# Kernel tuning notes

Measured on AMD Instinct MI355X. Metric: run time of the kernel, lower is better.

## Reference

```python
import jax, jax.numpy as jnp
import numpy as np

N_EMBD = 2048
N_HEAD = 16
HEAD_DIM = N_EMBD // N_HEAD
B, T = 8, 1024
EPS = 1e-5


def setup_inputs() -> dict:
    key = jax.random.key(0)
    ks = jax.random.split(key, 8)
    s = 0.02
    return {
        "x": jax.random.normal(ks[0], (B, T, N_EMBD), dtype=jnp.float32),
        "ln1_w": jnp.ones((N_EMBD,), jnp.float32),
        "ln1_b": jnp.zeros((N_EMBD,), jnp.float32),
        "qkv_w": jax.random.normal(ks[1], (3 * N_EMBD, N_EMBD), jnp.float32) * s,
        "qkv_b": jnp.zeros((3 * N_EMBD,), jnp.float32),
        "out_w": jax.random.normal(ks[2], (N_EMBD, N_EMBD), jnp.float32) * s,
        "out_b": jnp.zeros((N_EMBD,), jnp.float32),
        "ln2_w": jnp.ones((N_EMBD,), jnp.float32),
        "ln2_b": jnp.zeros((N_EMBD,), jnp.float32),
        "fc1_w": jax.random.normal(ks[3], (4 * N_EMBD, N_EMBD), jnp.float32) * s,
        "fc1_b": jnp.zeros((4 * N_EMBD,), jnp.float32),
        "fc2_w": jax.random.normal(ks[4], (N_EMBD, 4 * N_EMBD), jnp.float32) * s,
        "fc2_b": jnp.zeros((N_EMBD,), jnp.float32),
    }


def _layernorm(x, w, b):
    mu = jnp.mean(x, axis=-1, keepdims=True)
    var = jnp.var(x, axis=-1, keepdims=True)
    return (x - mu) * jax.lax.rsqrt(var + EPS) * w + b


def _attention(x, qkv_w, qkv_b, out_w, out_b):
    Bb, Tt, C = x.shape
    qkv = x @ qkv_w.T + qkv_b                      # [B,T,3C]
    q, k, v = jnp.split(qkv, 3, axis=-1)
    def heads(t):  # [B,T,C] -> [B,H,T,D]
        return t.reshape(Bb, Tt, N_HEAD, HEAD_DIM).transpose(0, 2, 1, 3)
    q, k, v = heads(q), heads(k), heads(v)
    scale = 1.0 / np.sqrt(HEAD_DIM).astype(np.float32)
    scores = jnp.einsum('bhqd,bhkd->bhqk', q, k) * scale
    causal = jnp.tril(jnp.ones((Tt, Tt), dtype=bool))
    scores = jnp.where(causal, scores, -jnp.inf)
    attn = jax.nn.softmax(scores, axis=-1)         # dropout p=0 -> identity
    out = jnp.einsum('bhqk,bhkd->bhqd', attn, v)
    out = out.transpose(0, 2, 1, 3).reshape(Bb, Tt, C)
    return out @ out_w.T + out_b


def _mlp(x, fc1_w, fc1_b, fc2_w, fc2_b):
    h = jax.nn.gelu(x @ fc1_w.T + fc1_b, approximate=False)  # torch GELU is exact erf
    return h @ fc2_w.T + fc2_b


def reference(x, ln1_w, ln1_b, qkv_w, qkv_b, out_w, out_b,
              ln2_w, ln2_b, fc1_w, fc1_b, fc2_w, fc2_b):
    x = x + _attention(_layernorm(x, ln1_w, ln1_b), qkv_w, qkv_b, out_w, out_b)
    x = x + _mlp(_layernorm(x, ln2_w, ln2_b), fc1_w, fc1_b, fc2_w, fc2_b)
    return x
```

## Files before the change

kernel.cpp:

```cpp
#include <hip/hip_runtime.h>
#include <hip/hip_bf16.h>

typedef __attribute__((ext_vector_type(8))) short short8;
typedef __attribute__((ext_vector_type(4))) short short4v;
typedef __attribute__((ext_vector_type(4))) float f32x4;
typedef __attribute__((address_space(3))) char lds_char;

static __device__ __forceinline__ ushort f2bf(float f) {
  union { __hip_bfloat16 h; ushort u; } cv;
  cv.h = __float2bfloat16(f);
  return cv.u;
}

#define GLOAD_LDS16(gp, lp)                                            \
  __builtin_amdgcn_global_load_lds(                                    \
      (const __attribute__((address_space(1))) void*)(gp),             \
      (__attribute__((address_space(3))) void*)(lp), 16, 0, 0)

#define BAR   asm volatile("s_barrier" ::: "memory")
#define VM0   asm volatile("s_waitcnt vmcnt(0)" ::: "memory")
#define LGKM0_SB do { asm volatile("s_waitcnt lgkmcnt(0)" ::: "memory");  \
                      __builtin_amdgcn_sched_barrier(0); } while (0)

__global__ __launch_bounds__(256) void cvt_all_k(const float* __restrict__ w0, ushort* __restrict__ o0, int n0,
                                                 const float* __restrict__ w1, ushort* __restrict__ o1, int n1,
                                                 const float* __restrict__ w2, ushort* __restrict__ o2, int n2,
                                                 const float* __restrict__ w3, ushort* __restrict__ o3, int n3) {
  int i = blockIdx.x * 256 + threadIdx.x;
  const float* in; ushort* out;
  if (i < n0)           { in = w0; out = o0; }
  else if (i < n0 + n1) { i -= n0; in = w1; out = o1; }
  else if (i < n0 + n1 + n2) { i -= n0 + n1; in = w2; out = o2; }
  else                  { i -= n0 + n1 + n2; if (i >= n3) return; in = w3; out = o3; }
  const float4* p = (const float4*)in + (size_t)i * 2;
  float4 a = p[0], b = p[1];
  short8 o;
  o[0] = f2bf(a.x); o[1] = f2bf(a.y); o[2] = f2bf(a.z); o[3] = f2bf(a.w);
  o[4] = f2bf(b.x); o[5] = f2bf(b.y); o[6] = f2bf(b.z); o[7] = f2bf(b.w);
  ((short8*)out)[i] = o;
}

__global__ __launch_bounds__(256) void ln_k(const float* __restrict__ x, const float* __restrict__ w,
                                            const float* __restrict__ b, ushort* __restrict__ o) {
  const int row = blockIdx.x, t = threadIdx.x;
  const float* xr = x + (size_t)row * 2048;
  float4 v0 = *(const float4*)(xr + t * 4);
  float4 v1 = *(const float4*)(xr + t * 4 + 1024);
  float s  = v0.x + v0.y + v0.z + v0.w + v1.x + v1.y + v1.z + v1.w;
  float s2 = v0.x*v0.x + v0.y*v0.y + v0.z*v0.z + v0.w*v0.w
           + v1.x*v1.x + v1.y*v1.y + v1.z*v1.z + v1.w*v1.w;
  #pragma unroll
  for (int m = 32; m; m >>= 1) { s += __shfl_xor(s, m); s2 += __shfl_xor(s2, m); }
  __shared__ float red[8];
  const int lane = t & 63, wv = t >> 6;
  if (lane == 0) { red[wv * 2] = s; red[wv * 2 + 1] = s2; }
  __syncthreads();
  s  = red[0] + red[2] + red[4] + red[6];
  s2 = red[1] + red[3] + red[5] + red[7];
  const float mu = s * (1.f / 2048.f);
  const float rstd = rsqrtf(s2 * (1.f / 2048.f) - mu * mu + 1e-5f);
  float4 w0 = *(const float4*)(w + t * 4), w1 = *(const float4*)(w + t * 4 + 1024);
  float4 b0 = *(const float4*)(b + t * 4), b1 = *(const float4*)(b + t * 4 + 1024);
  short4v o0, o1;
  o0[0] = f2bf((v0.x - mu) * rstd * w0.x + b0.x);
  o0[1] = f2bf((v0.y - mu) * rstd * w0.y + b0.y);
  o0[2] = f2bf((v0.z - mu) * rstd * w0.z + b0.z);
  o0[3] = f2bf((v0.w - mu) * rstd * w0.w + b0.w);
  o1[0] = f2bf((v1.x - mu) * rstd * w1.x + b1.x);
  o1[1] = f2bf((v1.y - mu) * rstd * w1.y + b1.y);
  o1[2] = f2bf((v1.z - mu) * rstd * w1.z + b1.z);
  o1[3] = f2bf((v1.w - mu) * rstd * w1.w + b1.w);
  *(short4v*)(o + (size_t)row * 2048 + t * 4) = o0;
  *(short4v*)(o + (size_t)row * 2048 + t * 4 + 1024) = o1;
}

template <int EPI>
__global__ __launch_bounds__(512, 4) void gemm256_k(const ushort* __restrict__ A, const ushort* __restrict__ B,
                                                    const float* __restrict__ bias, const float* __restrict__ res,
                                                    void* __restrict__ outp, int M, int N, int K) {
  __shared__ __align__(16) char lds[49152];
  const int nbn = N >> 7;
  const int nwg = gridDim.x;
  const int cpx = nwg >> 3;
  const int bid = (blockIdx.x & 7) * cpx + (blockIdx.x >> 3);
  const int gsz = nbn << 2;
  const int g = bid / gsz, rr = bid % gsz;
  const int bm = (g << 2) + (rr & 3), bn = rr >> 2;
  const int m0 = bm << 8, n0 = bn << 7;
  const int t = threadIdx.x, lane = t & 63, wid = t >> 6;
  const int wr = wid >> 2, wcn = wid & 3;
  const int hi = lane >> 4, lo = lane & 15;
  const int srow = lane >> 3, sc8 = lane & 7;
  const int gcs = (sc8 ^ srow) * 8;
  const ushort* Abase = A + (size_t)m0 * K;
  const ushort* Bbase = B + (size_t)n0 * K;
  f32x4 acc[8][2] = {};

  auto stageA = [&](int h, int tt) {
    const size_t kof = (size_t)tt * 64 + gcs;
    #pragma unroll
    for (int j = 0; j < 2; j++) {
      const int rb = h * 128 + wid * 16 + j * 8;
      GLOAD_LDS16(Abase + (size_t)(rb + srow) * K + kof, (ushort*)(lds + rb * 128));
    }
  };
  auto stageB = [&](int tt) {
    const size_t kof = (size_t)tt * 64 + gcs;
    #pragma unroll
    for (int j = 0; j < 2; j++) {
      const int rb = wid * 16 + j * 8;
      GLOAD_LDS16(Bbase + (size_t)(rb + srow) * K + kof, (ushort*)(lds + 32768 + rb * 128));
    }
  };

  const int swz = (lo & 7) << 4;
  const char* LA = lds;
  const char* LB = lds + 32768;
  const int arow0 = wr * 128 + lo;
  const int brow0 = wcn * 32 + lo;

  const int NT = K >> 6;
  stageA(0, 0); stageA(1, 0); stageB(0);

  for (int tt = 0; tt < NT; ++tt) {
    VM0; BAR;
    __builtin_amdgcn_s_setprio(1);
    #pragma unroll
    for (int kk = 0; kk < 2; kk++) {
      const int cb = kk * 64 + hi * 16;
      short8 bb0 = *(const short8*)(LB + (brow0 + 0)  * 128 + (cb ^ swz));
      short8 bb1 = *(const short8*)(LB + (brow0 + 16) * 128 + (cb ^ swz));
      #pragma unroll
      for (int m = 0; m < 8; m++) {
        short8 af = *(const short8*)(LA + (arow0 + m * 16) * 128 + (cb ^ swz));
        acc[m][0] = __builtin_amdgcn_mfma_f32_16x16x32_bf16(af, bb0, acc[m][0], 0, 0, 0);
        acc[m][1] = __builtin_amdgcn_mfma_f32_16x16x32_bf16(af, bb1, acc[m][1], 0, 0, 0);
      }
    }
    __builtin_amdgcn_s_setprio(0);
    BAR;
    if (tt + 1 < NT) { stageA(0, tt + 1); stageA(1, tt + 1); stageB(tt + 1); }
  }

  #pragma unroll
  for (int m = 0; m < 8; m++) {
    const int grow = m0 + wr * 128 + m * 16 + hi * 4;
    #pragma unroll
    for (int ni = 0; ni < 2; ni++) {
      const int gcol = n0 + wcn * 32 + ni * 16 + lo;
      const float bv = bias[gcol];
      #pragma unroll
      for (int r = 0; r < 4; r++) {
        const size_t idx = (size_t)(grow + r) * N + gcol;
        float v = acc[m][ni][r] + bv;
        if constexpr (EPI == 0) ((ushort*)outp)[idx] = f2bf(v);
        else if constexpr (EPI == 1) ((float*)outp)[idx] = res[idx] + v;
        else if constexpr (EPI == 2) ((ushort*)outp)[idx] = f2bf(0.5f * v * (1.f + erff(v * 0.70710678118f)));
        else ((float*)outp)[idx] += v;
      }
    }
  }
}

__global__ __launch_bounds__(256) void attn_k(const ushort* __restrict__ qkv, ushort* __restrict__ o) {
  const int qb = 15 - blockIdx.y;
  const int bh = blockIdx.x;
  const int bb = bh >> 4, h = bh & 15;
  const int t = threadIdx.x, lane = t & 63, w = t >> 6;
  const int hi = lane >> 4, lo = lane & 15;
  __shared__ __align__(16) char ldsK[64 * 256];
  __shared__ __align__(16) char ldsV[64 * 256];
  __shared__ __align__(16) char ldsP[4][16 * 128];
  const size_t base = (size_t)bb * 1024 * 6144;
  const int qrow_a = qb * 64 + w * 16 + lo;
  short8 qf[4];
  #pragma unroll
  for (int kk = 0; kk < 4; kk++)
    qf[kk] = *(const short8*)(qkv + base + (size_t)qrow_a * 6144 + h * 128 + kk * 32 + hi * 8);
  float ms[4], ls[4];
  f32x4 oacc[8] = {};
  #pragma unroll
  for (int r = 0; r < 4; r++) { ms[r] = -1e30f; ls[r] = 0.f; }
  const int wave_qmax = qb * 64 + w * 16 + 15;
  const uint vbase = (uint)(size_t)(lds_char*)ldsV + hi * 2048 + lo * 8;
  const int k_r4  = lane >> 4;
  const int v_kv4 = (lane >> 1) & 3;
  const int v_d0  = (lane >> 3) * 16 + (lane & 1) * 8;

  for (int kv0 = 0; kv0 <= qb * 64; kv0 += 64) {
    __syncthreads();
    #pragma unroll
    for (int j = 0; j < 4; j++) {
      const int rb = w * 16 + j * 4;
      const int r  = rb + k_r4;
      const int c16 = (lane & 15) ^ (r & 7);
      GLOAD_LDS16(qkv + base + (size_t)(kv0 + r) * 6144 + 2048 + h * 128 + c16 * 8,
                  ldsK + rb * 256);
    }
    #pragma unroll
    for (int j = 0; j < 4; j++) {
      const int g = w * 4 + j;
      GLOAD_LDS16(qkv + base + (size_t)(kv0 + g * 4 + v_kv4) * 6144 + 4096 + h * 128 + v_d0,
                  ldsV + g * 1024);
    }
    __syncthreads();
    if (kv0 > wave_qmax) continue;
    f32x4 s[4];
    #pragma unroll
    for (int nb = 0; nb < 4; nb++) {
      f32x4 z = {};
      const int krow = nb * 16 + lo;
      #pragma unroll
      for (int kk = 0; kk < 4; kk++) {
        const int cb = kk * 64 + hi * 16;
        short8 kf = *(const short8*)(ldsK + krow * 256 + (cb ^ ((krow & 7) << 4)));
        z = __builtin_amdgcn_mfma_f32_16x16x32_bf16(qf[kk], kf, z, 0, 0, 0);
      }
      s[nb] = z;
    }
    float corr[4];
    #pragma unroll
    for (int r = 0; r < 4; r++) {
      const int qrow = qb * 64 + w * 16 + hi * 4 + r;
      float mx = -1e30f;
      #pragma unroll
      for (int nb = 0; nb < 4; nb++) {
        const int kcol = kv0 + nb * 16 + lo;
        float sv = s[nb][r] * 0.08838834764831845f;
        sv = (kcol <= qrow) ? sv : -1e30f;
        s[nb][r] = sv;
        mx = fmaxf(mx, sv);
      }
      #pragma unroll
      for (int msk = 1; msk < 16; msk <<= 1) mx = fmaxf(mx, __shfl_xor(mx, msk));
      const float mnew = fmaxf(ms[r], mx);
      corr[r] = __expf(ms[r] - mnew);
      ms[r] = mnew;
      float rs = 0.f;
      #pragma unroll
      for (int nb = 0; nb < 4; nb++) {
        const float p = __expf(s[nb][r] - mnew);
        s[nb][r] = p; rs += p;
      }
      #pragma unroll
      for (int msk = 1; msk < 16; msk <<= 1) rs += __shfl_xor(rs, msk);
      ls[r] = ls[r] * corr[r] + rs;
    }
    #pragma unroll
    for (int nf = 0; nf < 8; nf++)
      #pragma unroll
      for (int r = 0; r < 4; r++) oacc[nf][r] *= corr[r];
    #pragma unroll
    for (int r = 0; r < 4; r++) {
      const int prow = hi * 4 + r;
      #pragma unroll
      for (int nb = 0; nb < 4; nb++) {
        const int pcol = nb * 16 + lo;
        *(short*)(ldsP[w] + prow * 128 + ((pcol * 2) ^ ((prow & 7) << 4))) = (short)f2bf(s[nb][r]);
      }
    }
    #pragma unroll
    for (int ks = 0; ks < 2; ks++) {
      short8 pf = *(const short8*)(ldsP[w] + lo * 128 + ((ks * 64 + hi * 16) ^ ((lo & 7) << 4)));
      short4v v0[8], v1[8];
      #pragma unroll
      for (int nf = 0; nf < 8; nf++) {
        const uint a0 = vbase + ks * 8192 + nf * 128;
        asm volatile("ds_read_b64_tr_b16 %0, %1" : "=v"(v0[nf]) : "v"(a0));
        asm volatile("ds_read_b64_tr_b16 %0, %1" : "=v"(v1[nf]) : "v"(a0 + 1024));
      }
      LGKM0_SB;
      #pragma unroll
      for (int nf = 0; nf < 8; nf++) {
        short8 vf = __builtin_shufflevector(v0[nf], v1[nf], 0, 1, 2, 3, 4, 5, 6, 7);
        oacc[nf] = __builtin_amdgcn_mfma_f32_16x16x32_bf16(pf, vf, oacc[nf], 0, 0, 0);
      }
    }
  }
  #pragma unroll
  for (int r = 0; r < 4; r++) {
    const float inv = 1.f / ls[r];
    const int qrow = qb * 64 + w * 16 + hi * 4 + r;
    ushort* orow = o + ((size_t)(bb * 1024 + qrow)) * 2048 + h * 128;
    #pragma unroll
    for (int nf = 0; nf < 8; nf++)
      orow[nf * 16 + lo] = f2bf(oacc[nf][r] * inv);
  }
}

extern "C" void kernel_launch(void* const* d_in, const int* in_sizes, int n_in,
                              void* d_out, int out_size, void* d_ws, size_t ws_size,
                              hipStream_t stream) {
  const float* x     = (const float*)d_in[0];
  const float* ln1w  = (const float*)d_in[1];
  const float* ln1b  = (const float*)d_in[2];
  const float* qkvw  = (const float*)d_in[3];
  const float* qkvb  = (const float*)d_in[4];
  const float* outw  = (const float*)d_in[5];
  const float* outb  = (const float*)d_in[6];
  const float* ln2w  = (const float*)d_in[7];
  const float* ln2b  = (const float*)d_in[8];
  const float* fc1w  = (const float*)d_in[9];
  const float* fc1b  = (const float*)d_in[10];
  const float* fc2w  = (const float*)d_in[11];
  const float* fc2b  = (const float*)d_in[12];
  float* out = (float*)d_out;

  char* ws = (char*)d_ws;
  ushort* qkvw_bf = (ushort*)(ws);
  ushort* outw_bf = (ushort*)(ws + 25165824);
  ushort* fc1w_bf = (ushort*)(ws + 33554432);
  ushort* fc2w_bf = (ushort*)(ws + 67108864);
  ushort* bufA    = (ushort*)(ws + 100663296);
  ushort* bufR    = (ushort*)(ws + 134217728);

  cvt_all_k<<<24576, 256, 0, stream>>>(qkvw, qkvw_bf, 1572864,
                                       outw, outw_bf, 524288,
                                       fc1w, fc1w_bf, 2097152,
                                       fc2w, fc2w_bf, 2097152);

  ln_k<<<8192, 256, 0, stream>>>(x, ln1w, ln1b, bufA);
  gemm256_k<0><<<1536, 512, 0, stream>>>(bufA, qkvw_bf, qkvb, nullptr, bufR, 8192, 6144, 2048);
  attn_k<<<dim3(128, 16), 256, 0, stream>>>(bufR, bufA);
  gemm256_k<1><<<512, 512, 0, stream>>>(bufA, outw_bf, outb, x, out, 8192, 2048, 2048);
  ln_k<<<8192, 256, 0, stream>>>(out, ln2w, ln2b, bufA);
  gemm256_k<2><<<2048, 512, 0, stream>>>(bufA, fc1w_bf, fc1b, nullptr, bufR, 8192, 8192, 2048);
  gemm256_k<3><<<512, 512, 0, stream>>>(bufR, fc2w_bf, fc2b, nullptr, out, 8192, 2048, 8192);
}
```

Before: 1.010 ms.

## Switch GEMM to 32x32x16 MFMA with 4 waves and larger per-wave tiles

Rewrites the shared GEMM kernel so each of 4 waves (256 threads) computes a 128x64 sub-tile with 32x32x16 bf16 MFMA instructions instead of 8 waves using 16x16x32 MFMA. Staging loops issue more loads per wave to fill the same 256x128x64 LDS tile, and the epilogue is remapped to the 32x32 accumulator layout. The larger MFMA shape reduces LDS fragment reads per FLOP, but it doubles the accumulator registers per wave and halves the waves available to hide latency.

```diff
diff --git a/kernel.cpp b/kernel.cpp
--- a/kernel.cpp
+++ b/kernel.cpp
@@ -4,6 +4,7 @@
 typedef __attribute__((ext_vector_type(8))) short short8;
 typedef __attribute__((ext_vector_type(4))) short short4v;
 typedef __attribute__((ext_vector_type(4))) float f32x4;
+typedef __attribute__((ext_vector_type(16))) float f32x16;
 typedef __attribute__((address_space(3))) char lds_char;
 
 static __device__ __forceinline__ ushort f2bf(float f) {
@@ -75,9 +76,9 @@
 }
 
 template <int EPI>
-__global__ __launch_bounds__(512, 4) void gemm256_k(const ushort* __restrict__ A, const ushort* __restrict__ B,
-                                                    const float* __restrict__ bias, const float* __restrict__ res,
-                                                    void* __restrict__ outp, int M, int N, int K) {
+__global__ __launch_bounds__(256, 3) void gemm32_k(const ushort* __restrict__ A, const ushort* __restrict__ B,
+                                                   const float* __restrict__ bias, const float* __restrict__ res,
+                                                   void* __restrict__ outp, int M, int N, int K) {
   __shared__ __align__(16) char lds[49152];
   const int nbn = N >> 7;
   const int nwg = gridDim.x;
@@ -88,71 +89,71 @@
   const int bm = (g << 2) + (rr & 3), bn = rr >> 2;
   const int m0 = bm << 8, n0 = bn << 7;
   const int t = threadIdx.x, lane = t & 63, wid = t >> 6;
-  const int wr = wid >> 2, wcn = wid & 3;
-  const int hi = lane >> 4, lo = lane & 15;
+  const int wr = wid >> 1, wc = wid & 1;
+  const int r32 = lane & 31, kg = lane >> 5;
   const int srow = lane >> 3, sc8 = lane & 7;
   const int gcs = (sc8 ^ srow) * 8;
   const ushort* Abase = A + (size_t)m0 * K;
   const ushort* Bbase = B + (size_t)n0 * K;
-  f32x4 acc[8][2] = {};
-
-  auto stageA = [&](int h, int tt) {
+  f32x16 acc[4][2] = {};
+
+  auto stageA = [&](int tt) {
     const size_t kof = (size_t)tt * 64 + gcs;
     #pragma unroll
-    for (int j = 0; j < 2; j++) {
-      const int rb = h * 128 + wid * 16 + j * 8;
+    for (int j = 0; j < 8; j++) {
+      const int rb = wid * 64 + j * 8;
       GLOAD_LDS16(Abase + (size_t)(rb + srow) * K + kof, (ushort*)(lds + rb * 128));
     }
   };
   auto stageB = [&](int tt) {
     const size_t kof = (size_t)tt * 64 + gcs;
     #pragma unroll
-    for (int j = 0; j < 2; j++) {
-      const int rb = wid * 16 + j * 8;
+    for (int j = 0; j < 4; j++) {
+      const int rb = wid * 32 + j * 8;
       GLOAD_LDS16(Bbase + (size_t)(rb + srow) * K + kof, (ushort*)(lds + 32768 + rb * 128));
     }
   };
 
-  const int swz = (lo & 7) << 4;
-  const char* LA = lds;
-  const char* LB = lds + 32768;
-  const int arow0 = wr * 128 + lo;
-  const int brow0 = wcn * 32 + lo;
+  const int swz = (r32 & 7) << 4;
+  const char* LA = lds + (wr * 128 + r32) * 128;
+  const char* LB = lds + 32768 + (wc * 64 + r32) * 128;
+  const int kcol0 = kg * 16;
 
   const int NT = K >> 6;
-  stageA(0, 0); stageA(1, 0); stageB(0);
+  stageA(0); stageB(0);
 
   for (int tt = 0; tt < NT; ++tt) {
     VM0; BAR;
     __builtin_amdgcn_s_setprio(1);
     #pragma unroll
-    for (int kk = 0; kk < 2; kk++) {
-      const int cb = kk * 64 + hi * 16;
-      short8 bb0 = *(const short8*)(LB + (brow0 + 0)  * 128 + (cb ^ swz));
-      short8 bb1 = *(const short8*)(LB + (brow0 + 16) * 128 + (cb ^ swz));
-      #pragma unroll
-      for (int m = 0; m < 8; m++) {
-        short8 af = *(const short8*)(LA + (arow0 + m * 16) * 128 + (cb ^ swz));
-        acc[m][0] = __builtin_amdgcn_mfma_f32_16x16x32_bf16(af, bb0, acc[m][0], 0, 0, 0);
-        acc[m][1] = __builtin_amdgcn_mfma_f32_16x16x32_bf16(af, bb1, acc[m][1], 0, 0, 0);
+    for (int ks = 0; ks < 4; ks++) {
+      const int cb = (ks * 32 + kcol0) ^ swz;
+      short8 bf0 = *(const short8*)(LB + cb);
+      short8 bf1 = *(const short8*)(LB + 4096 + cb);
+      #pragma unroll
+      for (int m = 0; m < 4; m++) {
+        short8 af = *(const short8*)(LA + m * 4096 + cb);
+        acc[m][0] = __builtin_amdgcn_mfma_f32_32x32x16_bf16(af, bf0, acc[m][0], 0, 0, 0);
+        acc[m][1] = __builtin_amdgcn_mfma_f32_32x32x16_bf16(af, bf1, acc[m][1], 0, 0, 0);
       }
     }
     __builtin_amdgcn_s_setprio(0);
     BAR;
-    if (tt + 1 < NT) { stageA(0, tt + 1); stageA(1, tt + 1); stageB(tt + 1); }
+    if (tt + 1 < NT) { stageA(tt + 1); stageB(tt + 1); }
   }
 
   #pragma unroll
-  for (int m = 0; m < 8; m++) {
-    const int grow = m0 + wr * 128 + m * 16 + hi * 4;
-    #pragma unroll
-    for (int ni = 0; ni < 2; ni++) {
-      const int gcol = n0 + wcn * 32 + ni * 16 + lo;
+  for (int m = 0; m < 4; m++) {
+    const int gm = m0 + wr * 128 + m * 32 + 4 * kg;
+    #pragma unroll
+    for (int n = 0; n < 2; n++) {
+      const int gcol = n0 + wc * 64 + n * 32 + r32;
       const float bv = bias[gcol];
       #pragma unroll
-      for (int r = 0; r < 4; r++) {
-        const size_t idx = (size_t)(grow + r) * N + gcol;
-        float v = acc[m][ni][r] + bv;
+      for (int r = 0; r < 16; r++) {
+        const int grow = gm + (r & 3) + 8 * (r >> 2);
+        const size_t idx = (size_t)grow * N + gcol;
+        float v = acc[m][n][r] + bv;
         if constexpr (EPI == 0) ((ushort*)outp)[idx] = f2bf(v);
         else if constexpr (EPI == 1) ((float*)outp)[idx] = res[idx] + v;
         else if constexpr (EPI == 2) ((ushort*)outp)[idx] = f2bf(0.5f * v * (1.f + erff(v * 0.70710678118f)));
@@ -320,10 +321,10 @@
                                        fc2w, fc2w_bf, 2097152);
 
   ln_k<<<8192, 256, 0, stream>>>(x, ln1w, ln1b, bufA);
-  gemm256_k<0><<<1536, 512, 0, stream>>>(bufA, qkvw_bf, qkvb, nullptr, bufR, 8192, 6144, 2048);
+  gemm32_k<0><<<1536, 256, 0, stream>>>(bufA, qkvw_bf, qkvb, nullptr, bufR, 8192, 6144, 2048);
   attn_k<<<dim3(128, 16), 256, 0, stream>>>(bufR, bufA);
-  gemm256_k<1><<<512, 512, 0, stream>>>(bufA, outw_bf, outb, x, out, 8192, 2048, 2048);
+  gemm32_k<1><<<512, 256, 0, stream>>>(bufA, outw_bf, outb, x, out, 8192, 2048, 2048);
   ln_k<<<8192, 256, 0, stream>>>(out, ln2w, ln2b, bufA);
-  gemm256_k<2><<<2048, 512, 0, stream>>>(bufA, fc1w_bf, fc1b, nullptr, bufR, 8192, 8192, 2048);
-  gemm256_k<3><<<512, 512, 0, stream>>>(bufR, fc2w_bf, fc2b, nullptr, out, 8192, 2048, 8192);
-}
+  gemm32_k<2><<<2048, 256, 0, stream>>>(bufA, fc1w_bf, fc1b, nullptr, bufR, 8192, 8192, 2048);
+  gemm32_k<3><<<512, 256, 0, stream>>>(bufR, fc2w_bf, fc2b, nullptr, out, 8192, 2048, 8192);
+}
```

New measurement: 3.808 ms. 3.77x slower.
